# Performance work log

Hardware: AMD Instinct MI355X
Metric: run time of the kernel (lower is better)

Reference implementation:

```python
import jax, jax.numpy as jnp
from jax import lax
import numpy as np

VOCAB, TAGS, EMB, HID = 50000, 45, 256, 512
B, S = 32, 256


def setup_inputs() -> dict:
    key = jax.random.key(0)
    ks = jax.random.split(key, 12)
    sc = 0.05
    return {
        "x": jax.random.randint(ks[0], (B, S), 0, VOCAB),
        "tags": jax.random.randint(ks[1], (B, S), 0, TAGS),
        "emb": jax.random.normal(ks[2], (VOCAB, EMB), jnp.float32) * sc,
        "w_ih_f": jax.random.normal(ks[3], (4 * HID, EMB), jnp.float32) * sc,
        "w_hh_f": jax.random.normal(ks[4], (4 * HID, HID), jnp.float32) * sc,
        "b_f": jnp.zeros((4 * HID,), jnp.float32),
        "w_ih_b": jax.random.normal(ks[5], (4 * HID, EMB), jnp.float32) * sc,
        "w_hh_b": jax.random.normal(ks[6], (4 * HID, HID), jnp.float32) * sc,
        "b_b": jnp.zeros((4 * HID,), jnp.float32),
        "lin_w": jax.random.normal(ks[7], (TAGS, 2 * HID), jnp.float32) * sc,
        "lin_b": jnp.zeros((TAGS,), jnp.float32),
        "start_t": jax.random.normal(ks[8], (TAGS,), jnp.float32) * 0.1,
        "end_t": jax.random.normal(ks[9], (TAGS,), jnp.float32) * 0.1,
        "trans": jax.random.normal(ks[10], (TAGS,), jnp.float32)[:, None] * 0.0 + jax.random.normal(ks[11], (TAGS, TAGS), jnp.float32) * 0.1,
    }


def _lstm_dir(xs, w_ih, w_hh, b, reverse):
    # xs: [B,S,E]. PyTorch gate order: i, f, g, o.
    Bsz = xs.shape[0]
    H = w_hh.shape[1]
    def step(carry, x_t):
        h, c = carry
        g = x_t @ w_ih.T + h @ w_hh.T + b
        i, f, gg, o = jnp.split(g, 4, axis=-1)
        c = jax.nn.sigmoid(f) * c + jax.nn.sigmoid(i) * jnp.tanh(gg)
        h = jax.nn.sigmoid(o) * jnp.tanh(c)
        return (h, c), h
    init = (jnp.zeros((Bsz, H), xs.dtype), jnp.zeros((Bsz, H), xs.dtype))
    _, hs = lax.scan(step, init, jnp.swapaxes(xs, 0, 1), reverse=reverse)
    return jnp.swapaxes(hs, 0, 1)  # [B,S,H]


def _crf_nll(em, tags, start_t, end_t, trans):
    # em: [B,S,T]; numerator: score of gold path
    em_sc = jnp.take_along_axis(em, tags[..., None], axis=2)[..., 0].sum(axis=1)
    tr_sc = trans[tags[:, :-1], tags[:, 1:]].sum(axis=1)
    score = start_t[tags[:, 0]] + em_sc + tr_sc + end_t[tags[:, -1]]
    # partition function via forward algorithm (logsumexp recurrence)
    alpha0 = start_t + em[:, 0]  # [B,T]
    def step(alpha, e_t):
        alpha = jax.nn.logsumexp(alpha[:, :, None] + trans[None], axis=1) + e_t
        return alpha, None
    alpha, _ = lax.scan(step, alpha0, jnp.swapaxes(em[:, 1:], 0, 1))
    logZ = jax.nn.logsumexp(alpha + end_t, axis=1)
    return -(score - logZ).mean()  # reduction='mean', loss = -llh


def reference(x, tags, emb, w_ih_f, w_hh_f, b_f, w_ih_b, w_hh_b, b_b,
              lin_w, lin_b, start_t, end_t, trans):
    embeds = emb[x]                               # [B,S,E]
    h_f = _lstm_dir(embeds, w_ih_f, w_hh_f, b_f, False)
    h_b = _lstm_dir(embeds, w_ih_b, w_hh_b, b_b, True)
    lstm_out = jnp.concatenate([h_f, h_b], axis=-1)  # [B,S,2H]
    emissions = lstm_out @ lin_w.T + lin_b           # [B,S,T]
    return _crf_nll(emissions, tags, start_t, end_t, trans)
```

## Files before the change

### kernel.cpp

```cpp
#include <hip/hip_runtime.h>

#define BB 32
#define SS 256
#define EMBD 256
#define HIDD 512
#define NTAG 45
#define TPAD 48
#define NBLK 32
#define ROWS 64
#define APAD 520
#define GRID_REC 256

typedef __bf16 bf16x8 __attribute__((ext_vector_type(8)));
typedef float  f32x4  __attribute__((ext_vector_type(4)));
typedef short  s16x8  __attribute__((ext_vector_type(8)));
typedef short  s16x4  __attribute__((ext_vector_type(4)));

__device__ __forceinline__ unsigned short f2bf(float x) {
  unsigned u = __builtin_bit_cast(unsigned, x);
  u = (u + 0x7fffu + ((u >> 16) & 1u)) >> 16;
  return (unsigned short)u;
}
__device__ __forceinline__ float bf2f(unsigned short u) {
  unsigned v = ((unsigned)u) << 16; return __builtin_bit_cast(float, v);
}
__device__ __forceinline__ float ftanh(float x) {
  float e = __expf(2.f * x);
  return 1.f - 2.f / (e + 1.f);
}

__device__ __forceinline__ unsigned ld32_cpol(const unsigned* p, bool sys) {
  unsigned v;
  if (sys) asm volatile("global_load_dword %0, %1, off sc0 sc1\ns_waitcnt vmcnt(0)"
                        : "=v"(v) : "v"(p) : "memory");
  else     asm volatile("global_load_dword %0, %1, off sc0\ns_waitcnt vmcnt(0)"
                        : "=v"(v) : "v"(p) : "memory");
  return v;
}
__device__ __forceinline__ void st32_cpol(unsigned* p, unsigned v, bool sys) {
  if (sys) asm volatile("global_store_dword %0, %1, off sc0 sc1" :: "v"(p), "v"(v) : "memory");
  else     asm volatile("global_store_dword %0, %1, off sc0"     :: "v"(p), "v"(v) : "memory");
}
__device__ __forceinline__ unsigned ld32x2_cpol(const unsigned* p0, const unsigned* p1, bool sys) {
  unsigned a, b;
  if (sys) asm volatile("global_load_dword %0, %2, off sc0 sc1\n\t"
                        "global_load_dword %1, %3, off sc0 sc1\n\t"
                        "s_waitcnt vmcnt(0)"
                        : "=&v"(a), "=&v"(b) : "v"(p0), "v"(p1) : "memory");
  else     asm volatile("global_load_dword %0, %2, off sc0\n\t"
                        "global_load_dword %1, %3, off sc0\n\t"
                        "s_waitcnt vmcnt(0)"
                        : "=&v"(a), "=&v"(b) : "v"(p0), "v"(p1) : "memory");
  return a & b;
}

#define LD8(CPOL)                                                           \
  asm volatile("global_load_dwordx4 %0, %[q0], off " CPOL "\n\t"            \
               "global_load_dwordx4 %1, %[q1], off " CPOL "\n\t"            \
               "global_load_dwordx4 %2, %[q2], off " CPOL "\n\t"            \
               "global_load_dwordx4 %3, %[q3], off " CPOL "\n\t"            \
               "global_load_dwordx4 %4, %[q4], off " CPOL "\n\t"            \
               "global_load_dwordx4 %5, %[q5], off " CPOL "\n\t"            \
               "global_load_dwordx4 %6, %[q6], off " CPOL "\n\t"            \
               "global_load_dwordx4 %7, %[q7], off " CPOL "\n\t"            \
               "s_waitcnt vmcnt(0)"                                         \
               : "=&v"(v0), "=&v"(v1), "=&v"(v2), "=&v"(v3),                \
                 "=&v"(v4), "=&v"(v5), "=&v"(v6), "=&v"(v7)                 \
               : [q0] "v"(p), [q1] "v"(p + 2048), [q2] "v"(p + 4096),       \
                 [q3] "v"(p + 6144), [q4] "v"(p + 8192), [q5] "v"(p + 10240),\
                 [q6] "v"(p + 12288), [q7] "v"(p + 14336)                   \
               : "memory")

__global__ void k_pack_e(const int* __restrict__ x, const float* __restrict__ emb,
                         unsigned short* __restrict__ E) {
  int idx = blockIdx.x * 256 + threadIdx.x;
  int e = idx & 255; int bt = idx >> 8; int b = bt & 31; int t = bt >> 5;
  int tok = x[b * SS + t];
  E[idx] = f2bf(emb[(long)tok * EMBD + e]);
}

__global__ void k_pack_w(const float* __restrict__ wih_f, const float* __restrict__ whh_f,
                         const float* __restrict__ bf_,  const float* __restrict__ wih_b,
                         const float* __restrict__ whh_b, const float* __restrict__ bb_,
                         unsigned short* __restrict__ Wh, unsigned short* __restrict__ Wie,
                         float* __restrict__ Bh) {
  long idx = (long)blockIdx.x * 256 + threadIdx.x;
  int k = (int)(idx % 768); long rest = idx / 768;
  int r2 = (int)(rest & 2047); int dir = (int)(rest >> 11);
  int blk = r2 >> 6, rl = r2 & 63, gate = rl >> 4, hl = rl & 15;
  int orig = gate * HIDD + blk * 16 + hl;
  const float* wih = dir ? wih_b : wih_f;
  const float* whh = dir ? whh_b : whh_f;
  if (k < HIDD) Wh[((long)(dir * 2048 + r2)) * 512 + k] = f2bf(whh[(long)orig * HIDD + k]);
  else          Wie[((long)(dir * 2048 + r2)) * 256 + (k - 512)] = f2bf(wih[(long)orig * EMBD + (k - 512)]);
  if (k == 0) {
    const float* bias = dir ? bb_ : bf_;
    Bh[dir * 2048 + r2] = bias[orig];
  }
}

__global__ void k_pack_l(const float* __restrict__ lin_w, const float* __restrict__ lin_b,
                         unsigned short* __restrict__ LW, float* __restrict__ LB) {
  int idx = blockIdx.x * 256 + threadIdx.x;
  if (idx < TPAD * 1024) {
    int tag = idx >> 10; int c = idx & 1023;
    LW[idx] = (tag < NTAG) ? f2bf(lin_w[tag * 1024 + c]) : (unsigned short)0;
  } else if (idx < TPAD * 1024 + TPAD) {
    int tag = idx - TPAD * 1024;
    LB[tag] = (tag < NTAG) ? lin_b[tag] : 0.f;
  }
}

__launch_bounds__(256)
__global__ void k_eproj(const unsigned short* __restrict__ E,
                        const unsigned short* __restrict__ Wie,
                        const float* __restrict__ Bh,
                        unsigned short* __restrict__ Ep) {
  __shared__ unsigned short W2[64 * 264];
  const int bx = blockIdx.x;
  const int tg = bx & 63, blk = (bx >> 6) & 31, dir = bx >> 11;
  const int tid = threadIdx.x;
  const int w = tid >> 6, lane = tid & 63;
  const int lm = lane & 15, quad = lane >> 4;

  {
    const unsigned short* src = Wie + ((long)(dir * 2048 + blk * 64)) * 256;
    for (int i = 0; i < 8; ++i) {
      int c = i * 256 + tid;
      int row = c >> 5, off = c & 31;
      *(s16x8*)&W2[row * 264 + off * 8] = *(const s16x8*)&src[row * 256 + off * 8];
    }
  }
  __syncthreads();

  f32x4 acc[2][4] = {};
#pragma unroll
  for (int kk = 0; kk < 8; ++kk) {
    s16x8 av[2];
#pragma unroll
    for (int sub = 0; sub < 2; ++sub)
      av[sub] = *(const s16x8*)&E[((long)(tg * 128 + w * 32 + sub * 16 + lm)) * 256 + kk * 32 + quad * 8];
#pragma unroll
    for (int sub = 0; sub < 2; ++sub)
#pragma unroll
      for (int n = 0; n < 4; ++n) {
        s16x8 bs = *(const s16x8*)&W2[(n * 16 + lm) * 264 + kk * 32 + quad * 8];
        acc[sub][n] = __builtin_amdgcn_mfma_f32_16x16x32_bf16(
            __builtin_bit_cast(bf16x8, av[sub]), __builtin_bit_cast(bf16x8, bs), acc[sub][n], 0, 0, 0);
      }
  }
  float bh[4];
#pragma unroll
  for (int n = 0; n < 4; ++n) bh[n] = Bh[dir * 2048 + blk * 64 + n * 16 + lm];

  const int t = tg * 4 + w;
#pragma unroll
  for (int sub = 0; sub < 2; ++sub)
#pragma unroll
    for (int n = 0; n < 4; ++n) {
      s16x4 pk;
#pragma unroll
      for (int r = 0; r < 4; ++r) pk[r] = (short)f2bf(acc[sub][n][r] + bh[n]);
      int tidc = (sub * 2 + (n >> 1)) * 64 + quad * 16 + lm;
      *(s16x4*)&Ep[(((long)(dir * 32 + blk) * SS + t) * 256 + tidc) * 8 + (n & 1) * 4] = pk;
    }
}

__launch_bounds__(256, 1)
__global__ void k_rec(const unsigned short* __restrict__ Wh,
                      const unsigned short* __restrict__ Ep,
                      unsigned short* __restrict__ H,
                      unsigned int* __restrict__ sync) {
  __shared__ unsigned short A_ls[32 * APAD];
  __shared__ float G_ls[32 * 66 + 4608];
  __shared__ int fast_ls;

  const int bx = blockIdx.x;
  const int role = bx & 7;
  if (role >= 2) return;
  const int dir = role;
  const int blk = bx >> 3;
  const int tid = threadIdx.x;
  const int w = tid >> 6, lane = tid & 63;
  const int lm = lane & 15, quad = lane >> 4;
  const int mt = w >> 1, nt = w & 1;

  unsigned int* det   = sync;
  unsigned int* flags = sync + 64;

  s16x8 wb[2][16];
  {
    const unsigned short* wsrc =
        Wh + ((long)(dir * 2048 + blk * 64 + nt * 32 + lm)) * 512 + quad * 8;
#pragma unroll
    for (int ns = 0; ns < 2; ++ns)
#pragma unroll
      for (int kk = 0; kk < 16; ++kk)
        wb[ns][kk] = *(const s16x8*)&wsrc[ns * 16 * 512 + kk * 32];
  }

  unsigned xcc;
  asm volatile("s_getreg_b32 %0, hwreg(HW_REG_XCC_ID)" : "=s"(xcc));
  if (tid == 0) st32_cpol(&det[dir * 32 + blk], xcc | 0x100u, true);
  if (w == 0) {
    unsigned v;
    for (;;) {
      v = (lane < 32) ? ld32_cpol(&det[dir * 32 + lane], true) : (xcc | 0x100u);
      if (__ballot(v != 0u) == ~0ull) break;
      __builtin_amdgcn_s_sleep(1);
    }
    if (lane == 0) fast_ls = (__ballot(v == (xcc | 0x100u)) == ~0ull) ? 1 : 0;
  }
  __syncthreads();
  const bool fast = (fast_ls != 0);
  __threadfence();

  const int gb = tid >> 3, hp = tid & 7;
  float c0 = 0.f, c1 = 0.f;

  unsigned short* Hd = H + (long)dir * SS * BB * HIDD;
  unsigned int* flagd = flags + dir * SS * NBLK * 4;
  const unsigned short* Epd = Ep + (long)(dir * 32 + blk) * SS * 2048;

  s16x8 ecur = *(const s16x8*)&Epd[((long)(dir ? (SS - 1) : 0) * 256 + tid) * 8];
  s16x8 enext;

  for (int t = 0; t < SS; ++t) {
    f32x4 acc0 = {0.f, 0.f, 0.f, 0.f}, acc1 = {0.f, 0.f, 0.f, 0.f};
    if (t > 0) {
      if (w == 0) {
        const unsigned int* fl = flagd + (long)(t - 1) * (NBLK * 4);
        for (;;) {
          unsigned f = ld32x2_cpol(&fl[lane], &fl[lane + 64], !fast);
          if (__ballot(f != 0u) == ~0ull) break;
          __builtin_amdgcn_s_sleep(1);
        }
      }
      __syncthreads();
      {
        const int hslot = (dir == 0) ? (t - 1) : (SS - t);
        const unsigned short* p = Hd + (long)hslot * BB * HIDD + w * 512 + lane * 8;
        s16x8 v0, v1, v2, v3, v4, v5, v6, v7;
        if (fast) { LD8("sc0"); } else { LD8("sc0 sc1"); }
        unsigned short* d = &A_ls[w * APAD + lane * 8];
        *(s16x8*)(d + 0 * 2080) = v0; *(s16x8*)(d + 1 * 2080) = v1;
        *(s16x8*)(d + 2 * 2080) = v2; *(s16x8*)(d + 3 * 2080) = v3;
        *(s16x8*)(d + 4 * 2080) = v4; *(s16x8*)(d + 5 * 2080) = v5;
        *(s16x8*)(d + 6 * 2080) = v6; *(s16x8*)(d + 7 * 2080) = v7;
      }
      __syncthreads();
      {
        int tn = (t < SS - 1) ? t + 1 : t;
        int tEn = (dir == 0) ? tn : (SS - 1 - tn);
        enext = *(const s16x8*)&Epd[((long)tEn * 256 + tid) * 8];
      }
#pragma unroll
      for (int kk = 0; kk < 16; ++kk) {
        s16x8 av = *(const s16x8*)&A_ls[(mt * 16 + lm) * APAD + kk * 32 + quad * 8];
        acc0 = __builtin_amdgcn_mfma_f32_16x16x32_bf16(
            __builtin_bit_cast(bf16x8, av), __builtin_bit_cast(bf16x8, wb[0][kk]), acc0, 0, 0, 0);
        acc1 = __builtin_amdgcn_mfma_f32_16x16x32_bf16(
            __builtin_bit_cast(bf16x8, av), __builtin_bit_cast(bf16x8, wb[1][kk]), acc1, 0, 0, 0);
      }
    } else {
      int tEn = (dir == 0) ? 1 : (SS - 2);
      enext = *(const s16x8*)&Epd[((long)tEn * 256 + tid) * 8];
    }
#pragma unroll
    for (int r = 0; r < 4; ++r) {
      int mm = mt * 16 + quad * 4 + r;
      G_ls[mm * 66 + nt * 32 + lm]      = acc0[r] + bf2f((unsigned short)ecur[r]);
      G_ls[mm * 66 + nt * 32 + 16 + lm] = acc1[r] + bf2f((unsigned short)ecur[4 + r]);
    }
    __syncthreads();
    {
      float gi0 = G_ls[gb * 66 + 0  + 2 * hp], gi1 = G_ls[gb * 66 + 0  + 2 * hp + 1];
      float gf0 = G_ls[gb * 66 + 16 + 2 * hp], gf1 = G_ls[gb * 66 + 16 + 2 * hp + 1];
      float gg0 = G_ls[gb * 66 + 32 + 2 * hp], gg1 = G_ls[gb * 66 + 32 + 2 * hp + 1];
      float go0 = G_ls[gb * 66 + 48 + 2 * hp], go1 = G_ls[gb * 66 + 48 + 2 * hp + 1];
      float si0 = 1.f / (1.f + __expf(-gi0)), si1 = 1.f / (1.f + __expf(-gi1));
      float sf0 = 1.f / (1.f + __expf(-gf0)), sf1 = 1.f / (1.f + __expf(-gf1));
      float so0 = 1.f / (1.f + __expf(-go0)), so1 = 1.f / (1.f + __expf(-go1));
      float tg0 = ftanh(gg0), tg1 = ftanh(gg1);
      c0 = sf0 * c0 + si0 * tg0;
      c1 = sf1 * c1 + si1 * tg1;
      float h0 = so0 * ftanh(c0), h1 = so1 * ftanh(c1);
      int tslot = (dir == 0) ? t : (SS - 1 - t);
      unsigned hv = (unsigned)f2bf(h0) | ((unsigned)f2bf(h1) << 16);
      st32_cpol((unsigned*)&Hd[(long)tslot * BB * HIDD + (long)gb * HIDD + blk * 16 + 2 * hp],
                hv, !fast);
    }
    asm volatile("s_waitcnt vmcnt(0)" ::: "memory");
    if (t < SS - 1 && lane == 0)
      st32_cpol(&flagd[(long)t * (NBLK * 4) + blk * 4 + w], 1u, !fast);
    ecur = enext;
  }
}

__launch_bounds__(256)
__global__ void k_emis(const unsigned short* __restrict__ H,
                       const unsigned short* __restrict__ LW,
                       const float* __restrict__ LB,
                       float* __restrict__ EM) {
  const int row0 = blockIdx.x * 32;
  const int tid = threadIdx.x;
  const int w = tid >> 6, lane = tid & 63;
  const int lm = lane & 15, quad = lane >> 4;
  const unsigned short* Hf = H;
  const unsigned short* Hb = H + (long)SS * BB * HIDD;

  for (int tile = w; tile < 6; tile += 4) {
    int mt = tile / 3, nt = tile % 3;
    int arow = row0 + mt * 16 + lm;
    int nrow = nt * 16 + lm;
    f32x4 acc = {0.f, 0.f, 0.f, 0.f};
#pragma unroll 4
    for (int kk = 0; kk < 32; ++kk) {
      int k0 = kk * 32 + quad * 8;
      s16x8 asv = (k0 < HIDD) ? *(const s16x8*)&Hf[(long)arow * HIDD + k0]
                              : *(const s16x8*)&Hb[(long)arow * HIDD + (k0 - HIDD)];
      s16x8 bsv = *(const s16x8*)&LW[nrow * 1024 + k0];
      acc = __builtin_amdgcn_mfma_f32_16x16x32_bf16(
          __builtin_bit_cast(bf16x8, asv), __builtin_bit_cast(bf16x8, bsv), acc, 0, 0, 0);
    }
    float bias = LB[nrow];
#pragma unroll
    for (int r = 0; r < 4; ++r) {
      int mm = row0 + mt * 16 + quad * 4 + r;
      EM[(long)mm * TPAD + nrow] = acc[r] + bias;
    }
  }
}

__global__ void k_crf(const int* __restrict__ tags, const float* __restrict__ start_t,
                      const float* __restrict__ end_t, const float* __restrict__ trans,
                      const float* __restrict__ EM, float* __restrict__ chain) {
  __shared__ float T_ls[NTAG * TPAD];
  __shared__ float ET[48 * 48 + 16];
  __shared__ float P_ls[64];
  const int b = blockIdx.x;
  const int lane = threadIdx.x;
  const int j = lane;

  for (int i = lane; i < NTAG * NTAG; i += 64)
    T_ls[(i / NTAG) * TPAD + (i % NTAG)] = trans[i];
  for (int i = lane; i < 48 * 48 + 16; i += 64) ET[i] = 0.f;
  __syncthreads();

  float Mj = -1e30f;
  if (j < NTAG) {
    for (int i = 0; i < NTAG; ++i) Mj = fmaxf(Mj, T_ls[i * TPAD + j]);
    for (int i = 0; i < NTAG; ++i) ET[i * 48 + j] = __expf(T_ls[i * TPAD + j] - Mj);
  }
  __syncthreads();

  float et[48];
#pragma unroll
  for (int i = 0; i < 48; ++i) et[i] = ET[i * 48 + j];

  float part = 0.f;
  for (int t = lane; t < SS; t += 64) {
    int tg = tags[b * SS + t];
    part += EM[((long)t * BB + b) * TPAD + tg];
    if (t + 1 < SS) part += T_ls[tg * TPAD + tags[b * SS + t + 1]];
    if (t == 0)      part += start_t[tg];
    if (t == SS - 1) part += end_t[tg];
  }
  for (int off = 32; off; off >>= 1) part += __shfl_down(part, off);
  float score = __shfl(part, 0);

  float alpha = (j < NTAG) ? (start_t[j] + EM[(long)b * TPAD + j]) : -1e30f;
  float e_next = (j < NTAG) ? EM[((long)BB + b) * TPAD + j] : 0.f;
  for (int t = 1; t < SS; ++t) {
    float e_cur = e_next;
    if (t < SS - 1) e_next = (j < NTAG) ? EM[((long)(t + 1) * BB + b) * TPAD + j] : 0.f;
    float am = alpha;
#pragma unroll
    for (int off = 32; off; off >>= 1) am = fmaxf(am, __shfl_xor(am, off));
    float p = __expf(alpha - am);
    P_ls[lane] = p;
    __builtin_amdgcn_wave_barrier();
    float s0 = 0.f, s1 = 0.f, s2 = 0.f, s3 = 0.f;
#pragma unroll
    for (int i0 = 0; i0 < 48; i0 += 4) {
      f32x4 pv = *(const f32x4*)&P_ls[i0];
      s0 += pv.x * et[i0];
      s1 += pv.y * et[i0 + 1];
      s2 += pv.z * et[i0 + 2];
      s3 += pv.w * et[i0 + 3];
    }
    __builtin_amdgcn_wave_barrier();
    float s = (s0 + s1) + (s2 + s3);
    float na = am + Mj + __logf(s) + e_cur;
    alpha = (j < NTAG) ? na : -1e30f;
  }
  float v = (j < NTAG) ? (alpha + end_t[j]) : -1e30f;
  float mx = v;
  for (int off = 32; off; off >>= 1) mx = fmaxf(mx, __shfl_xor(mx, off));
  float s = __expf(v - mx);
  for (int off = 32; off; off >>= 1) s += __shfl_xor(s, off);
  if (lane == 0) chain[b] = score - (mx + __logf(s));
}

__global__ void k_fin(const float* __restrict__ chain, float* __restrict__ out) {
  int lane = threadIdx.x;
  float v = (lane < BB) ? chain[lane] : 0.f;
  for (int off = 32; off; off >>= 1) v += __shfl_xor(v, off);
  if (lane == 0) out[0] = -v / (float)BB;
}

extern "C" void kernel_launch(void* const* d_in, const int* in_sizes, int n_in,
                              void* d_out, int out_size, void* d_ws, size_t ws_size,
                              hipStream_t stream) {
  const int*   x      = (const int*)d_in[0];
  const int*   tags   = (const int*)d_in[1];
  const float* emb    = (const float*)d_in[2];
  const float* wih_f  = (const float*)d_in[3];
  const float* whh_f  = (const float*)d_in[4];
  const float* b_f    = (const float*)d_in[5];
  const float* wih_b  = (const float*)d_in[6];
  const float* whh_b  = (const float*)d_in[7];
  const float* b_b    = (const float*)d_in[8];
  const float* lin_w  = (const float*)d_in[9];
  const float* lin_b  = (const float*)d_in[10];
  const float* start_t= (const float*)d_in[11];
  const float* end_t  = (const float*)d_in[12];
  const float* trans  = (const float*)d_in[13];

  char* ws = (char*)d_ws;
  size_t off = 0;
  auto alloc = [&](size_t bytes) {
    void* p = ws + off; off = (off + bytes + 255) & ~(size_t)255; return p;
  };
  size_t sync_bytes = (64 + 2 * SS * NBLK * 4) * 4;
  unsigned int*   sync = (unsigned int*) alloc(sync_bytes);
  unsigned short* E   = (unsigned short*)alloc((size_t)SS * BB * EMBD * 2);
  unsigned short* Wh  = (unsigned short*)alloc((size_t)2 * 2048 * 512 * 2);
  unsigned short* Wie = (unsigned short*)alloc((size_t)2 * 2048 * 256 * 2);
  float*          Bh  = (float*)         alloc((size_t)2 * 2048 * 4);
  unsigned short* Ep  = (unsigned short*)alloc((size_t)2 * 32 * SS * 2048 * 2);
  unsigned short* H   = (unsigned short*)alloc((size_t)2 * SS * BB * HIDD * 2);
  unsigned short* LW  = (unsigned short*)alloc((size_t)TPAD * 1024 * 2);
  float*          LB  = (float*)         alloc((size_t)TPAD * 4);
  float*          EM  = (float*)         alloc((size_t)SS * BB * TPAD * 4);
  float*          chain = (float*)       alloc((size_t)BB * 4);

  hipMemsetAsync(sync, 0, sync_bytes, stream);
  k_pack_e<<<dim3((SS * BB * EMBD) / 256), dim3(256), 0, stream>>>(x, emb, E);
  k_pack_w<<<dim3((2 * 2048 * 768) / 256), dim3(256), 0, stream>>>(
      wih_f, whh_f, b_f, wih_b, whh_b, b_b, Wh, Wie, Bh);
  k_pack_l<<<dim3((TPAD * 1024 + TPAD + 255) / 256), dim3(256), 0, stream>>>(
      lin_w, lin_b, LW, LB);
  k_eproj<<<dim3(4096), dim3(256), 0, stream>>>(E, Wie, Bh, Ep);

  void* kargs[] = {&Wh, &Ep, &H, &sync};
  hipLaunchCooperativeKernel((const void*)k_rec, dim3(GRID_REC), dim3(256), kargs, 0, stream);

  k_emis<<<dim3((SS * BB) / 32), dim3(256), 0, stream>>>(H, LW, LB, EM);
  k_crf<<<dim3(BB), dim3(64), 0, stream>>>(tags, start_t, end_t, trans, EM, chain);
  k_fin<<<dim3(1), dim3(64), 0, stream>>>(chain, (float*)d_out);
}
```

Baseline: 1.175 ms.

## Split recurrence flag polling per wave and drop a block-wide barrier

Each wave now polls only the 32 step flags for the producer blocks whose hidden-state columns it needs. It then loads just that 128-column slice for all 32 batch rows, instead of wave 0 polling every flag and then a __syncthreads releasing everyone. This removes one block barrier per timestep and lets waves start loading as soon as their own producers finish. The prefetch of the next step's input projection moves to after the flag store, which may hide less of its latency.

```diff
diff --git a/kernel.cpp b/kernel.cpp
--- a/kernel.cpp
+++ b/kernel.cpp
@@ -40,18 +40,6 @@
 __device__ __forceinline__ void st32_cpol(unsigned* p, unsigned v, bool sys) {
   if (sys) asm volatile("global_store_dword %0, %1, off sc0 sc1" :: "v"(p), "v"(v) : "memory");
   else     asm volatile("global_store_dword %0, %1, off sc0"     :: "v"(p), "v"(v) : "memory");
-}
-__device__ __forceinline__ unsigned ld32x2_cpol(const unsigned* p0, const unsigned* p1, bool sys) {
-  unsigned a, b;
-  if (sys) asm volatile("global_load_dword %0, %2, off sc0 sc1\n\t"
-                        "global_load_dword %1, %3, off sc0 sc1\n\t"
-                        "s_waitcnt vmcnt(0)"
-                        : "=&v"(a), "=&v"(b) : "v"(p0), "v"(p1) : "memory");
-  else     asm volatile("global_load_dword %0, %2, off sc0\n\t"
-                        "global_load_dword %1, %3, off sc0\n\t"
-                        "s_waitcnt vmcnt(0)"
-                        : "=&v"(a), "=&v"(b) : "v"(p0), "v"(p1) : "memory");
-  return a & b;
 }
 
 #define LD8(CPOL)                                                           \
@@ -223,37 +211,31 @@
   const unsigned short* Epd = Ep + (long)(dir * 32 + blk) * SS * 2048;
 
   s16x8 ecur = *(const s16x8*)&Epd[((long)(dir ? (SS - 1) : 0) * 256 + tid) * 8];
-  s16x8 enext;
 
   for (int t = 0; t < SS; ++t) {
     f32x4 acc0 = {0.f, 0.f, 0.f, 0.f}, acc1 = {0.f, 0.f, 0.f, 0.f};
     if (t > 0) {
-      if (w == 0) {
-        const unsigned int* fl = flagd + (long)(t - 1) * (NBLK * 4);
+      {
+        const unsigned int* fl = flagd + (long)(t - 1) * (NBLK * 4) + w * 32;
         for (;;) {
-          unsigned f = ld32x2_cpol(&fl[lane], &fl[lane + 64], !fast);
+          unsigned f = (lane < 32) ? ld32_cpol(&fl[lane], !fast) : 1u;
           if (__ballot(f != 0u) == ~0ull) break;
           __builtin_amdgcn_s_sleep(1);
         }
       }
-      __syncthreads();
       {
         const int hslot = (dir == 0) ? (t - 1) : (SS - t);
-        const unsigned short* p = Hd + (long)hslot * BB * HIDD + w * 512 + lane * 8;
+        const unsigned short* p =
+            Hd + (long)hslot * BB * HIDD + (lane >> 4) * HIDD + w * 128 + (lane & 15) * 8;
         s16x8 v0, v1, v2, v3, v4, v5, v6, v7;
         if (fast) { LD8("sc0"); } else { LD8("sc0 sc1"); }
-        unsigned short* d = &A_ls[w * APAD + lane * 8];
+        unsigned short* d = &A_ls[(lane >> 4) * APAD + w * 128 + (lane & 15) * 8];
         *(s16x8*)(d + 0 * 2080) = v0; *(s16x8*)(d + 1 * 2080) = v1;
         *(s16x8*)(d + 2 * 2080) = v2; *(s16x8*)(d + 3 * 2080) = v3;
         *(s16x8*)(d + 4 * 2080) = v4; *(s16x8*)(d + 5 * 2080) = v5;
         *(s16x8*)(d + 6 * 2080) = v6; *(s16x8*)(d + 7 * 2080) = v7;
       }
       __syncthreads();
-      {
-        int tn = (t < SS - 1) ? t + 1 : t;
-        int tEn = (dir == 0) ? tn : (SS - 1 - tn);
-        enext = *(const s16x8*)&Epd[((long)tEn * 256 + tid) * 8];
-      }
 #pragma unroll
       for (int kk = 0; kk < 16; ++kk) {
         s16x8 av = *(const s16x8*)&A_ls[(mt * 16 + lm) * APAD + kk * 32 + quad * 8];
@@ -262,9 +244,6 @@
         acc1 = __builtin_amdgcn_mfma_f32_16x16x32_bf16(
             __builtin_bit_cast(bf16x8, av), __builtin_bit_cast(bf16x8, wb[1][kk]), acc1, 0, 0, 0);
       }
-    } else {
-      int tEn = (dir == 0) ? 1 : (SS - 2);
-      enext = *(const s16x8*)&Epd[((long)tEn * 256 + tid) * 8];
     }
 #pragma unroll
     for (int r = 0; r < 4; ++r) {
@@ -291,9 +270,12 @@
                 hv, !fast);
     }
     asm volatile("s_waitcnt vmcnt(0)" ::: "memory");
-    if (t < SS - 1 && lane == 0)
-      st32_cpol(&flagd[(long)t * (NBLK * 4) + blk * 4 + w], 1u, !fast);
-    ecur = enext;
+    if (t < SS - 1) {
+      if (lane == 0)
+        st32_cpol(&flagd[(long)t * (NBLK * 4) + blk * 4 + w], 1u, !fast);
+      int tEn = (dir == 0) ? (t + 1) : (SS - 2 - t);
+      ecur = *(const s16x8*)&Epd[((long)tEn * 256 + tid) * 8];
+    }
   }
 }
 
```

Measured after the change: 1.526 ms. 29.9% more time.
